# Kernel tuning notes

Hardware: AMD Instinct MI355X
Metric: run time of the kernel (lower is better)

Reference implementation:

```python
import jax, jax.numpy as jnp
import numpy as np

B, S = 32, 2048
D = 128      # embedding_dim
H = 256      # hidden_dim
K = 512      # codebook_size
RECON_COEF, COMMIT_COEF, VQ_COEF = 1.0, 0.15, 0.05


def _conv1d(x, w, b):
    # x: [B, Cin, S], w: [Cout, Cin, 3], 'SAME' padding (padding=1, k=3)
    y = jax.lax.conv_general_dilated(x, w, window_strides=(1,), padding='SAME',
                                     dimension_numbers=('NCH', 'OIH', 'NCH'))
    return y + b[None, :, None]


def _lrelu(x):
    return jnp.where(x >= 0, x, 0.2 * x)


def setup_inputs() -> dict:
    key = jax.random.key(0)
    ks = jax.random.split(key, 14)

    def w(k, shape, fan_in):
        bound = 1.0 / np.sqrt(fan_in)
        return jax.random.uniform(k, shape, jnp.float32, -bound, bound)

    return {
        'x': jax.random.normal(ks[0], (B, S), jnp.float32),
        'codebook': jax.random.normal(ks[1], (K, D), jnp.float32),
        'ew1': w(ks[2], (H, 1, 3), 1 * 3),  'eb1': w(ks[3], (H,), 1 * 3),
        'ew2': w(ks[4], (H, H, 3), H * 3),  'eb2': w(ks[5], (H,), H * 3),
        'ew3': w(ks[6], (D, H, 3), H * 3),  'eb3': w(ks[7], (D,), H * 3),
        'dw1': w(ks[8], (H, D, 3), D * 3),  'db1': w(ks[9], (H,), D * 3),
        'dw2': w(ks[10], (H, H, 3), H * 3), 'db2': w(ks[11], (H,), H * 3),
        'dw3': w(ks[12], (1, H, 3), H * 3), 'db3': w(ks[13], (1,), H * 3),
    }


def reference(x, codebook, ew1, eb1, ew2, eb2, ew3, eb3, dw1, db1, dw2, db2, dw3, db3):
    # ---- encode ----
    h = x[:, None, :]                                  # [B,1,S]
    h = _lrelu(_conv1d(h, ew1, eb1))
    h = _lrelu(_conv1d(h, ew2, eb2))
    z = _conv1d(h, ew3, eb3)                           # [B,D,S]

    # ---- vector quantize (eval mode: no EMA update) ----
    zt = jnp.transpose(z, (0, 2, 1))                   # [B,S,D]
    z_flat = zt.reshape(-1, D)                         # [B*S,D]
    # squared distances: |z|^2 + |c|^2 - 2 z c^T
    d = (jnp.sum(z_flat ** 2, axis=1, keepdims=True)
         + jnp.sum(codebook ** 2, axis=1)
         - 2.0 * z_flat @ codebook.T)                  # [B*S,K]
    idx = jnp.argmin(d, axis=1)                        # [B*S]
    z_q = codebook[idx].reshape(zt.shape)              # [B,S,D] (== one-hot @ codebook)

    vq_loss = jnp.mean((jax.lax.stop_gradient(zt) - z_q) ** 2) * VQ_COEF
    commitment_loss = jnp.mean((zt - jax.lax.stop_gradient(z_q)) ** 2) * COMMIT_COEF
    indices = idx.reshape(B, S)

    # ---- decode ----
    h = jnp.transpose(z_q, (0, 2, 1))                  # [B,D,S]
    h = _lrelu(_conv1d(h, dw1, db1))
    h = _lrelu(_conv1d(h, dw2, db2))
    x_recon = _conv1d(h, dw3, db3)[:, 0, :]            # [B,S]

    recon_loss = jnp.mean((x - x_recon) ** 2) * RECON_COEF
    loss = recon_loss + vq_loss + commitment_loss
    return x_recon, indices, loss, recon_loss, vq_loss, commitment_loss
```

## Files before the change

### kernel.cpp

```cpp
#include <hip/hip_runtime.h>
#include <float.h>

#define S_LEN 2048
#define BATCH 32
#define HCH   256
#define DCH   128
#define KCODES 512

typedef float  f32x4  __attribute__((ext_vector_type(4)));
typedef short  bf16x8 __attribute__((ext_vector_type(8)));
typedef short  short8 __attribute__((ext_vector_type(8)));

__device__ __forceinline__ float lrelu_f(float v) { return v >= 0.f ? v : 0.2f * v; }

__device__ __forceinline__ short f2bf(float f) {
    unsigned u = __float_as_uint(f);
    u = u + 0x7fffu + ((u >> 16) & 1u);
    return (short)(u >> 16);
}
__device__ __forceinline__ float bf2f(unsigned short u) {
    return __uint_as_float(((unsigned)u) << 16);
}

__global__ void prep_cb_split_kernel(const float* __restrict__ cb,
                                     short* __restrict__ cb_hi, short* __restrict__ cb_lo,
                                     float* __restrict__ cnorm) {
    int k = blockIdx.x * 256 + threadIdx.x;
    if (k < KCODES) {
        float s = 0.f;
        for (int d = 0; d < DCH; ++d) {
            float v = cb[k * DCH + d];
            s += v * v;
            short hi = f2bf(v);
            short lo = f2bf(v - bf2f((unsigned short)hi));
            cb_hi[k * DCH + d] = hi;
            cb_lo[k * DCH + d] = lo;
        }
        cnorm[k] = s;
    }
}

__global__ void prep_w_split_kernel(const float* __restrict__ Wsrc,
                                    short* __restrict__ Wh, short* __restrict__ Wl,
                                    int Cout, int Cin) {
    int i = blockIdx.x * 256 + threadIdx.x;
    int total = 3 * Cout * Cin;
    if (i < total) {
        int t = i / (Cout * Cin);
        int rem = i - t * Cout * Cin;
        int co = rem / Cin;
        int ci = rem - co * Cin;
        float v = Wsrc[(co * Cin + ci) * 3 + t];
        short hi = f2bf(v);
        Wh[i] = hi;
        Wl[i] = f2bf(v - bf2f((unsigned short)hi));
    }
}

__global__ void prep_wdec_kernel(const float* __restrict__ Wsrc, short* __restrict__ Wdst,
                                 int Cin) {
    int i = blockIdx.x * 256 + threadIdx.x;
    int total = 3 * 256 * Cin;
    if (i < total) {
        int t = i / (256 * Cin);
        int rem = i - t * 256 * Cin;
        int co = rem / Cin;
        int ci = rem - co * Cin;
        Wdst[i] = f2bf(Wsrc[(co * Cin + ci) * 3 + t]);
    }
}

__global__ void prep_w3t_kernel(const float* __restrict__ w3, float* __restrict__ w3t) {
    int i = blockIdx.x * 256 + threadIdx.x;
    if (i < 768) {
        int t = i / 256, ci = i - t * 256;
        w3t[i] = w3[ci * 3 + t];
    }
}

__global__ __launch_bounds__(256) void enc_conv1_cl_kernel(
        const float* __restrict__ x, short* __restrict__ h_hi, short* __restrict__ h_lo,
        const float* __restrict__ w, const float* __restrict__ bias) {
    __shared__ float ws[HCH * 3];
    __shared__ float bs[HCH];
    int tid = threadIdx.x;
    for (int i = tid; i < HCH * 3; i += 256) ws[i] = w[i];
    for (int i = tid; i < HCH; i += 256) bs[i] = bias[i];
    __syncthreads();
    int b = blockIdx.y;
    int s = blockIdx.x * 32 + (tid >> 3);
    int cch = tid & 7;
    const float* xb = x + (size_t)b * S_LEN;
    float xm = (s > 0) ? xb[s - 1] : 0.f;
    float x0 = xb[s];
    float xp = (s < S_LEN - 1) ? xb[s + 1] : 0.f;
    size_t base = ((size_t)(b * S_LEN + s)) * HCH + cch * 32;
#pragma unroll
    for (int cc = 0; cc < 4; ++cc) {
        short8 oh, ol;
#pragma unroll
        for (int e = 0; e < 8; ++e) {
            int co = cch * 32 + cc * 8 + e;
            float v = ws[co * 3 + 0] * xm + ws[co * 3 + 1] * x0 + ws[co * 3 + 2] * xp + bs[co];
            v = lrelu_f(v);
            short hi = f2bf(v);
            oh[e] = hi;
            ol[e] = f2bf(v - bf2f((unsigned short)hi));
        }
        *(short8*)(h_hi + base + cc * 8) = oh;
        *(short8*)(h_lo + base + cc * 8) = ol;
    }
}

__global__ __launch_bounds__(256) void conv_mfma_split(
        const short* __restrict__ in_hi, const short* __restrict__ in_lo,
        short* __restrict__ out_hi, short* __restrict__ out_lo,
        const short* __restrict__ wt_hi, const short* __restrict__ wt_lo,
        const float* __restrict__ bias, int Cin, int Cout, int do_lrelu) {
    __shared__ short smem[20800];
    short* Xh = smem;
    short* Xl = smem + 130 * 40;

    const int tid = threadIdx.x;
    const int lane = tid & 63;
    const int w = tid >> 6;
    const int m = lane & 15;
    const int q = lane >> 4;
    const int sOff = (w & 1) * 64;
    const int cOff = (w >> 1) * 64;
    const int b = blockIdx.z;
    const int s0 = blockIdx.x * 128;
    const int co0 = blockIdx.y * 128;

    f32x4 acc[4][4];
    f32x4 zero4 = {0.f, 0.f, 0.f, 0.f};
#pragma unroll
    for (int i = 0; i < 4; ++i)
#pragma unroll
        for (int j = 0; j < 4; ++j) acc[i][j] = zero4;

    const short* inhb = in_hi + (size_t)b * S_LEN * Cin;
    const short* inlb = in_lo + (size_t)b * S_LEN * Cin;

    for (int ci0 = 0; ci0 < Cin; ci0 += 32) {
        __syncthreads();
        for (int c = tid; c < 520; c += 256) {
            int r = c >> 2, part = c & 3;
            int s = s0 - 1 + r;
            float4 vh = make_float4(0.f, 0.f, 0.f, 0.f);
            float4 vl = vh;
            if (s >= 0 && s < S_LEN) {
                size_t goff = (size_t)s * Cin + ci0 + part * 8;
                vh = *(const float4*)(inhb + goff);
                vl = *(const float4*)(inlb + goff);
            }
            *(float4*)(Xh + r * 40 + part * 8) = vh;
            *(float4*)(Xl + r * 40 + part * 8) = vl;
        }
        __syncthreads();

#pragma unroll
        for (int t = 0; t < 3; ++t) {
            bf16x8 ah[4], al[4], bh[4], bl[4];
#pragma unroll
            for (int i = 0; i < 4; ++i) {
                int row = sOff + i * 16 + m + t;
                ah[i] = *(const bf16x8*)(Xh + row * 40 + q * 8);
                al[i] = *(const bf16x8*)(Xl + row * 40 + q * 8);
            }
#pragma unroll
            for (int j = 0; j < 4; ++j) {
                size_t woff = ((size_t)(t * Cout + co0 + cOff + j * 16 + m)) * Cin + ci0 + q * 8;
                bh[j] = *(const bf16x8*)(wt_hi + woff);
                bl[j] = *(const bf16x8*)(wt_lo + woff);
            }
#pragma unroll
            for (int i = 0; i < 4; ++i)
#pragma unroll
                for (int j = 0; j < 4; ++j) {
                    acc[i][j] = __builtin_amdgcn_mfma_f32_16x16x32_bf16(ah[i], bh[j], acc[i][j], 0, 0, 0);
                    acc[i][j] = __builtin_amdgcn_mfma_f32_16x16x32_bf16(ah[i], bl[j], acc[i][j], 0, 0, 0);
                    acc[i][j] = __builtin_amdgcn_mfma_f32_16x16x32_bf16(al[i], bh[j], acc[i][j], 0, 0, 0);
                }
        }
    }

    short* obH = smem + w * 5120;
    short* obL = obH + 2560;
#pragma unroll
    for (int p = 0; p < 2; ++p) {
        __syncthreads();
#pragma unroll
        for (int jj = 0; jj < 2; ++jj) {
            int j = 2 * p + jj;
            float bv = bias[co0 + cOff + j * 16 + m];
#pragma unroll
            for (int i = 0; i < 4; ++i) {
#pragma unroll
                for (int r = 0; r < 4; ++r) {
                    float val = acc[i][j][r] + bv;
                    if (do_lrelu) val = lrelu_f(val);
                    short hi = f2bf(val);
                    short lo = f2bf(val - bf2f((unsigned short)hi));
                    int row = i * 16 + q * 4 + r;
                    int col = jj * 16 + m;
                    obH[row * 40 + col] = hi;
                    obL[row * 40 + col] = lo;
                }
            }
        }
        __syncthreads();
        const int chunk = lane & 3;
        const int rsub = lane >> 2;
#pragma unroll
        for (int it = 0; it < 4; ++it) {
            int row = it * 16 + rsub;
            short8 vh = *(const short8*)(obH + row * 40 + chunk * 8);
            short8 vl = *(const short8*)(obL + row * 40 + chunk * 8);
            size_t goff = ((size_t)(b * S_LEN + s0 + sOff + row)) * Cout + co0 + cOff + p * 32 + chunk * 8;
            *(short8*)(out_hi + goff) = vh;
            *(short8*)(out_lo + goff) = vl;
        }
    }
}

__global__ __launch_bounds__(256) void vq_mfma_kernel(
        const short* __restrict__ z_hi, const short* __restrict__ z_lo,
        const short* __restrict__ cb_hi, const short* __restrict__ cb_lo,
        const float* __restrict__ cnorm, int* __restrict__ idx_out,
        float* __restrict__ idx_f_out) {
    __shared__ short smem[2 * 64 * 136];
    __shared__ float redv[64][4];
    __shared__ int   redi[64][4];
    short* Zh = smem;
    short* Zl = smem + 64 * 136;

    const int tid = threadIdx.x;
    const int lane = tid & 63;
    const int w = tid >> 6;
    const int m = lane & 15;
    const int q = lane >> 4;
    const int n0 = blockIdx.x * 64;

    for (int c = tid; c < 2048; c += 256) {
        int buf = c >> 10;
        int rem = c & 1023;
        int r = rem >> 4, part = rem & 15;
        size_t goff = (size_t)(n0 + r) * DCH + part * 8;
        float4 v = buf ? *(const float4*)(z_lo + goff) : *(const float4*)(z_hi + goff);
        *(float4*)((buf ? Zl : Zh) + r * 136 + part * 8) = v;
    }
    __syncthreads();

    float best[4][4];
    int besti[4][4];
#pragma unroll
    for (int i = 0; i < 4; ++i)
#pragma unroll
        for (int r = 0; r < 4; ++r) { best[i][r] = FLT_MAX; besti[i][r] = 0; }

    for (int k0 = 0; k0 < KCODES; k0 += 256) {
        f32x4 acc[4][4];
        f32x4 zero4 = {0.f, 0.f, 0.f, 0.f};
#pragma unroll
        for (int i = 0; i < 4; ++i)
#pragma unroll
            for (int j = 0; j < 4; ++j) acc[i][j] = zero4;

#pragma unroll
        for (int d0 = 0; d0 < DCH; d0 += 32) {
            bf16x8 ah[4], al[4], bh[4], bl[4];
#pragma unroll
            for (int i = 0; i < 4; ++i) {
                int row = i * 16 + m;
                ah[i] = *(const bf16x8*)(Zh + row * 136 + d0 + q * 8);
                al[i] = *(const bf16x8*)(Zl + row * 136 + d0 + q * 8);
            }
#pragma unroll
            for (int j = 0; j < 4; ++j) {
                size_t coff = (size_t)(k0 + w * 64 + j * 16 + m) * DCH + d0 + q * 8;
                bh[j] = *(const bf16x8*)(cb_hi + coff);
                bl[j] = *(const bf16x8*)(cb_lo + coff);
            }
#pragma unroll
            for (int i = 0; i < 4; ++i)
#pragma unroll
                for (int j = 0; j < 4; ++j) {
                    acc[i][j] = __builtin_amdgcn_mfma_f32_16x16x32_bf16(ah[i], bh[j], acc[i][j], 0, 0, 0);
                    acc[i][j] = __builtin_amdgcn_mfma_f32_16x16x32_bf16(ah[i], bl[j], acc[i][j], 0, 0, 0);
                    acc[i][j] = __builtin_amdgcn_mfma_f32_16x16x32_bf16(al[i], bh[j], acc[i][j], 0, 0, 0);
                }
        }
#pragma unroll
        for (int j = 0; j < 4; ++j) {
            int k = k0 + w * 64 + j * 16 + m;
            float cn = cnorm[k];
#pragma unroll
            for (int i = 0; i < 4; ++i)
#pragma unroll
                for (int r = 0; r < 4; ++r) {
                    float dv = cn - 2.f * acc[i][j][r];
                    if (dv < best[i][r]) { best[i][r] = dv; besti[i][r] = k; }
                }
        }
    }

#pragma unroll
    for (int mask = 1; mask < 16; mask <<= 1) {
#pragma unroll
        for (int i = 0; i < 4; ++i)
#pragma unroll
            for (int r = 0; r < 4; ++r) {
                float ov = __shfl_xor(best[i][r], mask);
                int oi = __shfl_xor(besti[i][r], mask);
                if (ov < best[i][r] || (ov == best[i][r] && oi < besti[i][r])) {
                    best[i][r] = ov; besti[i][r] = oi;
                }
            }
    }
    if (m == 0) {
#pragma unroll
        for (int i = 0; i < 4; ++i)
#pragma unroll
            for (int r = 0; r < 4; ++r) {
                int srow = i * 16 + q * 4 + r;
                redv[srow][w] = best[i][r];
                redi[srow][w] = besti[i][r];
            }
    }
    __syncthreads();
    if (tid < 64) {
        float bv = redv[tid][0];
        int bi = redi[tid][0];
#pragma unroll
        for (int w2 = 1; w2 < 4; ++w2) {
            float v = redv[tid][w2];
            int ii = redi[tid][w2];
            if (v < bv || (v == bv && ii < bi)) { bv = v; bi = ii; }
        }
        int n = n0 + tid;
        idx_out[n] = bi;
        idx_f_out[n] = (float)bi;
    }
}

__global__ __launch_bounds__(256) void gather_vqsum_kernel(
        const float* __restrict__ cb, const int* __restrict__ idxb,
        const short* __restrict__ z_hi, const short* __restrict__ z_lo,
        short* __restrict__ zq, float* __restrict__ acc_vq) {
    int tid = threadIdx.x;
    int b = blockIdx.y;
    int s = blockIdx.x * 32 + (tid >> 3);
    int dpart = tid & 7;
    int n = b * S_LEN + s;
    int k = idxb[n];
    const float* src = cb + (size_t)k * DCH + dpart * 16;
    size_t zoff = (size_t)n * DCH + dpart * 16;
    float sum = 0.f;
    short8 outv[2];
#pragma unroll
    for (int half = 0; half < 2; ++half) {
        float4 f0 = *(const float4*)(src + half * 8);
        float4 f1 = *(const float4*)(src + half * 8 + 4);
        bf16x8 zh = *(const bf16x8*)(z_hi + zoff + half * 8);
        bf16x8 zl = *(const bf16x8*)(z_lo + zoff + half * 8);
        float qv[8] = {f0.x, f0.y, f0.z, f0.w, f1.x, f1.y, f1.z, f1.w};
        short8 o;
#pragma unroll
        for (int e = 0; e < 8; ++e) {
            o[e] = f2bf(qv[e]);
            float zv = bf2f((unsigned short)zh[e]) + bf2f((unsigned short)zl[e]);
            float df = zv - qv[e];
            sum += df * df;
        }
        outv[half] = o;
    }
    *(short8*)(zq + zoff) = outv[0];
    *(short8*)(zq + zoff + 8) = outv[1];
    for (int off = 32; off > 0; off >>= 1) sum += __shfl_down(sum, off);
    __shared__ float wsum[4];
    if ((tid & 63) == 0) wsum[tid >> 6] = sum;
    __syncthreads();
    if (tid == 0) atomicAdd(acc_vq, wsum[0] + wsum[1] + wsum[2] + wsum[3]);
}

__global__ __launch_bounds__(256) void conv_mfma_cl(
        const short* __restrict__ in, short* __restrict__ out,
        const short* __restrict__ wt, const float* __restrict__ bias,
        int Cin) {
    __shared__ short smem[24672];
    short* Xs = smem;
    short* Ws = smem + 130 * 48;

    const int tid = threadIdx.x;
    const int lane = tid & 63;
    const int w = tid >> 6;
    const int m = lane & 15;
    const int q = lane >> 4;
    const int sOff = (w & 1) * 64;
    const int cOff = (w >> 1) * 64;
    const int b = blockIdx.z;
    const int s0 = blockIdx.x * 128;
    const int co0 = blockIdx.y * 128;

    f32x4 acc[4][4];
    f32x4 zero4 = {0.f, 0.f, 0.f, 0.f};
#pragma unroll
    for (int i = 0; i < 4; ++i)
#pragma unroll
        for (int j = 0; j < 4; ++j) acc[i][j] = zero4;

    const short* inb = in + (size_t)b * S_LEN * Cin;

    for (int ci0 = 0; ci0 < Cin; ci0 += 32) {
        __syncthreads();
        for (int c = tid; c < 520; c += 256) {
            int r = c >> 2, part = c & 3;
            int s = s0 - 1 + r;
            float4 v = make_float4(0.f, 0.f, 0.f, 0.f);
            if (s >= 0 && s < S_LEN)
                v = *(const float4*)(inb + (size_t)s * Cin + ci0 + part * 8);
            *(float4*)(Xs + r * 48 + part * 8) = v;
        }
        for (int c = tid; c < 1536; c += 256) {
            int t = c >> 9;
            int rem = c & 511;
            int cr = rem >> 2, part = rem & 3;
            float4 v = *(const float4*)(wt + ((size_t)(t * 256 + co0 + cr)) * Cin + ci0 + part * 8);
            *(float4*)(Ws + (t * 128 + cr) * 48 + part * 8) = v;
        }
        __syncthreads();

#pragma unroll
        for (int t = 0; t < 3; ++t) {
            bf16x8 a[4], bb[4];
#pragma unroll
            for (int i = 0; i < 4; ++i)
                a[i] = *(const bf16x8*)(Xs + (sOff + i * 16 + m + t) * 48 + q * 8);
#pragma unroll
            for (int j = 0; j < 4; ++j)
                bb[j] = *(const bf16x8*)(Ws + (t * 128 + cOff + j * 16 + m) * 48 + q * 8);
#pragma unroll
            for (int i = 0; i < 4; ++i)
#pragma unroll
                for (int j = 0; j < 4; ++j)
                    acc[i][j] = __builtin_amdgcn_mfma_f32_16x16x32_bf16(
                        a[i], bb[j], acc[i][j], 0, 0, 0);
        }
    }

    __syncthreads();

    short* ob = smem + w * (64 * 80);
#pragma unroll
    for (int j = 0; j < 4; ++j) {
        float bv = bias[co0 + cOff + j * 16 + m];
#pragma unroll
        for (int i = 0; i < 4; ++i) {
#pragma unroll
            for (int r = 0; r < 4; ++r) {
                float val = acc[i][j][r] + bv;
                val = lrelu_f(val);
                ob[(i * 16 + q * 4 + r) * 80 + j * 16 + m] = f2bf(val);
            }
        }
    }
    const int rsel = lane >> 3;
    const int off8 = (lane & 7) * 8;
#pragma unroll
    for (int pass = 0; pass < 8; ++pass) {
        int rr = pass * 8 + rsel;
        short8 v = *(const short8*)(ob + rr * 80 + off8);
        *(short8*)(out + ((size_t)(b * S_LEN + s0 + sOff + rr)) * 256 + co0 + cOff + off8) = v;
    }
}

__global__ __launch_bounds__(256) void dec_conv3_tiled_kernel(
        const short* __restrict__ h, const float* __restrict__ w3t,
        const float* __restrict__ b3, const float* __restrict__ x,
        float* __restrict__ xr, float* __restrict__ acc_recon) {
    __shared__ short Zs[66 * 264];
    __shared__ float ws[3 * 256];
    __shared__ float wsum[4];
    int tid = threadIdx.x;
    int b = blockIdx.y;
    int s0 = blockIdx.x * 64;
    const short* hb = h + (size_t)b * S_LEN * HCH;
    for (int i = tid; i < 768; i += 256) ws[i] = w3t[i];
    for (int c = tid; c < 2112; c += 256) {
        int r = c >> 5, part = c & 31;
        int g = s0 - 1 + r;
        short8 v = {0, 0, 0, 0, 0, 0, 0, 0};
        if (g >= 0 && g < S_LEN)
            v = *(const short8*)(hb + (size_t)g * HCH + part * 8);
        *(short8*)(Zs + r * 264 + part * 8) = v;
    }
    __syncthreads();

    int quarter = tid & 3;
    int sl = tid >> 2;
    float a0 = 0.f, a1 = 0.f, a2 = 0.f, a3 = 0.f;
#pragma unroll
    for (int t = 0; t < 3; ++t) {
        const short* zrow = Zs + (sl + t) * 264 + quarter * 64;
        const float* wrow = ws + t * 256 + quarter * 64;
#pragma unroll
        for (int c = 0; c < 8; ++c) {
            bf16x8 v = *(const bf16x8*)(zrow + c * 8);
            float4 w0 = *(const float4*)(wrow + c * 8);
            float4 w1 = *(const float4*)(wrow + c * 8 + 4);
            a0 = fmaf(w0.x, bf2f((unsigned short)v[0]), a0);
            a1 = fmaf(w0.y, bf2f((unsigned short)v[1]), a1);
            a2 = fmaf(w0.z, bf2f((unsigned short)v[2]), a2);
            a3 = fmaf(w0.w, bf2f((unsigned short)v[3]), a3);
            a0 = fmaf(w1.x, bf2f((unsigned short)v[4]), a0);
            a1 = fmaf(w1.y, bf2f((unsigned short)v[5]), a1);
            a2 = fmaf(w1.z, bf2f((unsigned short)v[6]), a2);
            a3 = fmaf(w1.w, bf2f((unsigned short)v[7]), a3);
        }
    }
    float acc = (a0 + a1) + (a2 + a3);
    acc += __shfl_xor(acc, 1);
    acc += __shfl_xor(acc, 2);
    float df2 = 0.f;
    if (quarter == 0) {
        int s = s0 + sl;
        float tot = acc + b3[0];
        xr[b * S_LEN + s] = tot;
        float df = x[b * S_LEN + s] - tot;
        df2 = df * df;
    }
    for (int off = 32; off > 0; off >>= 1) df2 += __shfl_down(df2, off);
    int lane = tid & 63, wv = tid >> 6;
    if (lane == 0) wsum[wv] = df2;
    __syncthreads();
    if (tid == 0) atomicAdd(acc_recon, wsum[0] + wsum[1] + wsum[2] + wsum[3]);
}

__global__ void finalize_kernel(const float* __restrict__ accs, float* __restrict__ out) {
    if (threadIdx.x == 0) {
        float vqm = accs[0] / ((float)BATCH * S_LEN * DCH);
        float rm  = accs[1] / ((float)BATCH * S_LEN);
        float vq_loss = vqm * 0.05f;
        float commit  = vqm * 0.15f;
        float recon   = rm * 1.0f;
        out[0] = recon + vq_loss + commit;
        out[1] = recon;
        out[2] = vq_loss;
        out[3] = commit;
    }
}

extern "C" void kernel_launch(void* const* d_in, const int* in_sizes, int n_in,
                              void* d_out, int out_size, void* d_ws, size_t ws_size,
                              hipStream_t stream) {
    const float* x    = (const float*)d_in[0];
    const float* cb   = (const float*)d_in[1];
    const float* ew1  = (const float*)d_in[2];
    const float* eb1  = (const float*)d_in[3];
    const float* ew2  = (const float*)d_in[4];
    const float* eb2  = (const float*)d_in[5];
    const float* ew3  = (const float*)d_in[6];
    const float* eb3  = (const float*)d_in[7];
    const float* dw1  = (const float*)d_in[8];
    const float* db1  = (const float*)d_in[9];
    const float* dw2  = (const float*)d_in[10];
    const float* db2  = (const float*)d_in[11];
    const float* dw3  = (const float*)d_in[12];
    const float* db3  = (const float*)d_in[13];

    float* out = (float*)d_out;
    float* xr    = out;
    float* idx_f = out + BATCH * S_LEN;
    float* loss_out = out + 2 * BATCH * S_LEN;

    const size_t NH = (size_t)BATCH * S_LEN * HCH;
    const size_t ND = (size_t)BATCH * S_LEN * DCH;

    short* sp = (short*)d_ws;
    short* h1_hi = sp;
    short* h1_lo = sp + NH;
    short* z_hi  = sp;
    short* z_lo  = sp + ND;
    short* h1d_bf = sp;
    short* h2_hi = sp + 2 * NH;
    short* h2_lo = sp + 3 * NH;
    short* zq_bf = sp + 2 * NH;
    short* h2d_bf = sp + 3 * NH;
    short* sm = sp + 4 * NH;
    short* cb_hi = sm; sm += KCODES * DCH;
    short* cb_lo = sm; sm += KCODES * DCH;
    short* w2_hi = sm; sm += 3 * HCH * HCH;
    short* w2_lo = sm; sm += 3 * HCH * HCH;
    short* w3_hi = sm; sm += 3 * DCH * HCH;
    short* w3_lo = sm; sm += 3 * DCH * HCH;
    short* wbf_d1 = sm; sm += 3 * 256 * DCH;
    short* wbf_d2 = sm; sm += 3 * 256 * HCH;
    float* cnorm = (float*)sm;
    int* idxb = (int*)(cnorm + KCODES);
    float* w3t = (float*)(idxb + BATCH * S_LEN);
    float* accs = w3t + 768;

    hipMemsetAsync(accs, 0, 2 * sizeof(float), stream);

    prep_cb_split_kernel<<<2, 256, 0, stream>>>(cb, cb_hi, cb_lo, cnorm);
    prep_w_split_kernel<<<(3 * HCH * HCH + 255) / 256, 256, 0, stream>>>(ew2, w2_hi, w2_lo, HCH, HCH);
    prep_w_split_kernel<<<(3 * DCH * HCH + 255) / 256, 256, 0, stream>>>(ew3, w3_hi, w3_lo, DCH, HCH);
    prep_wdec_kernel<<<(3 * 256 * DCH + 255) / 256, 256, 0, stream>>>(dw1, wbf_d1, DCH);
    prep_wdec_kernel<<<(3 * 256 * HCH + 255) / 256, 256, 0, stream>>>(dw2, wbf_d2, HCH);
    prep_w3t_kernel<<<3, 256, 0, stream>>>(dw3, w3t);

    enc_conv1_cl_kernel<<<dim3(S_LEN / 32, BATCH), 256, 0, stream>>>(x, h1_hi, h1_lo, ew1, eb1);
    conv_mfma_split<<<dim3(S_LEN / 128, HCH / 128, BATCH), 256, 0, stream>>>(
        h1_hi, h1_lo, h2_hi, h2_lo, w2_hi, w2_lo, eb2, HCH, HCH, 1);
    conv_mfma_split<<<dim3(S_LEN / 128, DCH / 128, BATCH), 256, 0, stream>>>(
        h2_hi, h2_lo, z_hi, z_lo, w3_hi, w3_lo, eb3, HCH, DCH, 0);

    vq_mfma_kernel<<<(BATCH * S_LEN) / 64, 256, 0, stream>>>(
        z_hi, z_lo, cb_hi, cb_lo, cnorm, idxb, idx_f);
    gather_vqsum_kernel<<<dim3(S_LEN / 32, BATCH), 256, 0, stream>>>(
        cb, idxb, z_hi, z_lo, zq_bf, accs);

    conv_mfma_cl<<<dim3(S_LEN / 128, 2, BATCH), 256, 0, stream>>>(
        zq_bf, h1d_bf, wbf_d1, db1, DCH);
    conv_mfma_cl<<<dim3(S_LEN / 128, 2, BATCH), 256, 0, stream>>>(
        h1d_bf, h2d_bf, wbf_d2, db2, HCH);
    dec_conv3_tiled_kernel<<<dim3(S_LEN / 64, BATCH), 256, 0, stream>>>(
        h2d_bf, w3t, db3, x, xr, accs + 1);

    finalize_kernel<<<1, 64, 0, stream>>>(accs, loss_out);
}
```

Baseline: 524.7 us.

## Shrink conv LDS footprint, widen K-chunk to 64, read weights directly from global

Both MFMA conv kernels now stage 64 input channels per iteration with a padded stride of 68, which halves the number of barrier-separated load phases. The conv_mfma_cl kernel no longer stages weights in LDS and reads them straight from global/L2, as the split kernel already did. The epilogues write one 16-column chunk at a time through a small per-wave buffer, and launch_bounds now request 4 blocks per CU. Together these cut shared memory use to raise occupancy, at the cost of more global weight traffic and possible register pressure under the tighter bound. The VQ kernel also issues its codebook global loads before the LDS loads to hide their latency.

```diff
diff --git a/kernel.cpp b/kernel.cpp
--- a/kernel.cpp
+++ b/kernel.cpp
@@ -112,14 +112,14 @@
     }
 }
 
-__global__ __launch_bounds__(256) void conv_mfma_split(
+__global__ __launch_bounds__(256, 4) void conv_mfma_split(
         const short* __restrict__ in_hi, const short* __restrict__ in_lo,
         short* __restrict__ out_hi, short* __restrict__ out_lo,
         const short* __restrict__ wt_hi, const short* __restrict__ wt_lo,
         const float* __restrict__ bias, int Cin, int Cout, int do_lrelu) {
-    __shared__ short smem[20800];
+    __shared__ short smem[17680];
     short* Xh = smem;
-    short* Xl = smem + 130 * 40;
+    short* Xl = smem + 130 * 68;
 
     const int tid = threadIdx.x;
     const int lane = tid & 63;
@@ -142,82 +142,81 @@
     const short* inhb = in_hi + (size_t)b * S_LEN * Cin;
     const short* inlb = in_lo + (size_t)b * S_LEN * Cin;
 
-    for (int ci0 = 0; ci0 < Cin; ci0 += 32) {
+    for (int ci0 = 0; ci0 < Cin; ci0 += 64) {
         __syncthreads();
-        for (int c = tid; c < 520; c += 256) {
-            int r = c >> 2, part = c & 3;
+        for (int c = tid; c < 2080; c += 256) {
+            int r = c >> 4;
+            int sub = c & 15;
+            int half = sub >> 3;
+            int part = sub & 7;
             int s = s0 - 1 + r;
-            float4 vh = make_float4(0.f, 0.f, 0.f, 0.f);
-            float4 vl = vh;
+            float4 v = make_float4(0.f, 0.f, 0.f, 0.f);
             if (s >= 0 && s < S_LEN) {
                 size_t goff = (size_t)s * Cin + ci0 + part * 8;
-                vh = *(const float4*)(inhb + goff);
-                vl = *(const float4*)(inlb + goff);
-            }
-            *(float4*)(Xh + r * 40 + part * 8) = vh;
-            *(float4*)(Xl + r * 40 + part * 8) = vl;
+                v = half ? *(const float4*)(inlb + goff) : *(const float4*)(inhb + goff);
+            }
+            *(float4*)((half ? Xl : Xh) + r * 68 + part * 8) = v;
         }
         __syncthreads();
 
 #pragma unroll
-        for (int t = 0; t < 3; ++t) {
-            bf16x8 ah[4], al[4], bh[4], bl[4];
-#pragma unroll
-            for (int i = 0; i < 4; ++i) {
-                int row = sOff + i * 16 + m + t;
-                ah[i] = *(const bf16x8*)(Xh + row * 40 + q * 8);
-                al[i] = *(const bf16x8*)(Xl + row * 40 + q * 8);
-            }
-#pragma unroll
-            for (int j = 0; j < 4; ++j) {
-                size_t woff = ((size_t)(t * Cout + co0 + cOff + j * 16 + m)) * Cin + ci0 + q * 8;
-                bh[j] = *(const bf16x8*)(wt_hi + woff);
-                bl[j] = *(const bf16x8*)(wt_lo + woff);
-            }
-#pragma unroll
-            for (int i = 0; i < 4; ++i)
+        for (int ks = 0; ks < 2; ++ks) {
+            const int kofs = ks * 32;
+#pragma unroll
+            for (int t = 0; t < 3; ++t) {
+                bf16x8 ah[4], al[4], bh[4], bl[4];
 #pragma unroll
                 for (int j = 0; j < 4; ++j) {
-                    acc[i][j] = __builtin_amdgcn_mfma_f32_16x16x32_bf16(ah[i], bh[j], acc[i][j], 0, 0, 0);
-                    acc[i][j] = __builtin_amdgcn_mfma_f32_16x16x32_bf16(ah[i], bl[j], acc[i][j], 0, 0, 0);
-                    acc[i][j] = __builtin_amdgcn_mfma_f32_16x16x32_bf16(al[i], bh[j], acc[i][j], 0, 0, 0);
+                    size_t woff = ((size_t)(t * Cout + co0 + cOff + j * 16 + m)) * Cin + ci0 + kofs + q * 8;
+                    bh[j] = *(const bf16x8*)(wt_hi + woff);
+                    bl[j] = *(const bf16x8*)(wt_lo + woff);
                 }
-        }
-    }
-
-    short* obH = smem + w * 5120;
-    short* obL = obH + 2560;
-#pragma unroll
-    for (int p = 0; p < 2; ++p) {
-        __syncthreads();
-#pragma unroll
-        for (int jj = 0; jj < 2; ++jj) {
-            int j = 2 * p + jj;
-            float bv = bias[co0 + cOff + j * 16 + m];
-#pragma unroll
-            for (int i = 0; i < 4; ++i) {
-#pragma unroll
-                for (int r = 0; r < 4; ++r) {
-                    float val = acc[i][j][r] + bv;
-                    if (do_lrelu) val = lrelu_f(val);
-                    short hi = f2bf(val);
-                    short lo = f2bf(val - bf2f((unsigned short)hi));
-                    int row = i * 16 + q * 4 + r;
-                    int col = jj * 16 + m;
-                    obH[row * 40 + col] = hi;
-                    obL[row * 40 + col] = lo;
+#pragma unroll
+                for (int i = 0; i < 4; ++i) {
+                    int row = sOff + i * 16 + m + t;
+                    ah[i] = *(const bf16x8*)(Xh + row * 68 + kofs + q * 8);
+                    al[i] = *(const bf16x8*)(Xl + row * 68 + kofs + q * 8);
                 }
-            }
-        }
-        __syncthreads();
-        const int chunk = lane & 3;
-        const int rsub = lane >> 2;
-#pragma unroll
-        for (int it = 0; it < 4; ++it) {
-            int row = it * 16 + rsub;
-            short8 vh = *(const short8*)(obH + row * 40 + chunk * 8);
-            short8 vl = *(const short8*)(obL + row * 40 + chunk * 8);
-            size_t goff = ((size_t)(b * S_LEN + s0 + sOff + row)) * Cout + co0 + cOff + p * 32 + chunk * 8;
+#pragma unroll
+                for (int i = 0; i < 4; ++i)
+#pragma unroll
+                    for (int j = 0; j < 4; ++j) {
+                        acc[i][j] = __builtin_amdgcn_mfma_f32_16x16x32_bf16(ah[i], bh[j], acc[i][j], 0, 0, 0);
+                        acc[i][j] = __builtin_amdgcn_mfma_f32_16x16x32_bf16(ah[i], bl[j], acc[i][j], 0, 0, 0);
+                        acc[i][j] = __builtin_amdgcn_mfma_f32_16x16x32_bf16(al[i], bh[j], acc[i][j], 0, 0, 0);
+                    }
+            }
+        }
+    }
+
+    __syncthreads();
+    short* obH = smem + w * 2560;
+    short* obL = obH + 1280;
+#pragma unroll
+    for (int j = 0; j < 4; ++j) {
+        float bv = bias[co0 + cOff + j * 16 + m];
+#pragma unroll
+        for (int i = 0; i < 4; ++i) {
+#pragma unroll
+            for (int r = 0; r < 4; ++r) {
+                float val = acc[i][j][r] + bv;
+                if (do_lrelu) val = lrelu_f(val);
+                short hi = f2bf(val);
+                short lo = f2bf(val - bf2f((unsigned short)hi));
+                int row = i * 16 + q * 4 + r;
+                obH[row * 20 + m] = hi;
+                obL[row * 20 + m] = lo;
+            }
+        }
+        const int colchunk = lane & 1;
+        const int rbase = lane >> 1;
+#pragma unroll
+        for (int it = 0; it < 2; ++it) {
+            int row = it * 32 + rbase;
+            short8 vh = *(const short8*)(obH + row * 20 + colchunk * 8);
+            short8 vl = *(const short8*)(obL + row * 20 + colchunk * 8);
+            size_t goff = ((size_t)(b * S_LEN + s0 + sOff + row)) * Cout
+                        + co0 + cOff + j * 16 + colchunk * 8;
             *(short8*)(out_hi + goff) = vh;
             *(short8*)(out_lo + goff) = vl;
         }
@@ -271,16 +270,16 @@
         for (int d0 = 0; d0 < DCH; d0 += 32) {
             bf16x8 ah[4], al[4], bh[4], bl[4];
 #pragma unroll
+            for (int j = 0; j < 4; ++j) {
+                size_t coff = (size_t)(k0 + w * 64 + j * 16 + m) * DCH + d0 + q * 8;
+                bh[j] = *(const bf16x8*)(cb_hi + coff);
+                bl[j] = *(const bf16x8*)(cb_lo + coff);
+            }
+#pragma unroll
             for (int i = 0; i < 4; ++i) {
                 int row = i * 16 + m;
                 ah[i] = *(const bf16x8*)(Zh + row * 136 + d0 + q * 8);
                 al[i] = *(const bf16x8*)(Zl + row * 136 + d0 + q * 8);
-            }
-#pragma unroll
-            for (int j = 0; j < 4; ++j) {
-                size_t coff = (size_t)(k0 + w * 64 + j * 16 + m) * DCH + d0 + q * 8;
-                bh[j] = *(const bf16x8*)(cb_hi + coff);
-                bl[j] = *(const bf16x8*)(cb_lo + coff);
             }
 #pragma unroll
             for (int i = 0; i < 4; ++i)
@@ -384,13 +383,12 @@
     if (tid == 0) atomicAdd(acc_vq, wsum[0] + wsum[1] + wsum[2] + wsum[3]);
 }
 
-__global__ __launch_bounds__(256) void conv_mfma_cl(
+__global__ __launch_bounds__(256, 4) void conv_mfma_cl(
         const short* __restrict__ in, short* __restrict__ out,
         const short* __restrict__ wt, const float* __restrict__ bias,
         int Cin) {
-    __shared__ short smem[24672];
+    __shared__ short smem[8840];
     short* Xs = smem;
-    short* Ws = smem + 130 * 48;
 
     const int tid = threadIdx.x;
     const int lane = tid & 63;
@@ -412,46 +410,43 @@
 
     const short* inb = in + (size_t)b * S_LEN * Cin;
 
-    for (int ci0 = 0; ci0 < Cin; ci0 += 32) {
+    for (int ci0 = 0; ci0 < Cin; ci0 += 64) {
         __syncthreads();
-        for (int c = tid; c < 520; c += 256) {
-            int r = c >> 2, part = c & 3;
+        for (int c = tid; c < 1040; c += 256) {
+            int r = c >> 3;
+            int part = c & 7;
             int s = s0 - 1 + r;
             float4 v = make_float4(0.f, 0.f, 0.f, 0.f);
             if (s >= 0 && s < S_LEN)
                 v = *(const float4*)(inb + (size_t)s * Cin + ci0 + part * 8);
-            *(float4*)(Xs + r * 48 + part * 8) = v;
-        }
-        for (int c = tid; c < 1536; c += 256) {
-            int t = c >> 9;
-            int rem = c & 511;
-            int cr = rem >> 2, part = rem & 3;
-            float4 v = *(const float4*)(wt + ((size_t)(t * 256 + co0 + cr)) * Cin + ci0 + part * 8);
-            *(float4*)(Ws + (t * 128 + cr) * 48 + part * 8) = v;
+            *(float4*)(Xs + r * 68 + part * 8) = v;
         }
         __syncthreads();
 
 #pragma unroll
-        for (int t = 0; t < 3; ++t) {
-            bf16x8 a[4], bb[4];
-#pragma unroll
-            for (int i = 0; i < 4; ++i)
-                a[i] = *(const bf16x8*)(Xs + (sOff + i * 16 + m + t) * 48 + q * 8);
-#pragma unroll
-            for (int j = 0; j < 4; ++j)
-                bb[j] = *(const bf16x8*)(Ws + (t * 128 + cOff + j * 16 + m) * 48 + q * 8);
-#pragma unroll
-            for (int i = 0; i < 4; ++i)
+        for (int ks = 0; ks < 2; ++ks) {
+            const int kofs = ks * 32;
+#pragma unroll
+            for (int t = 0; t < 3; ++t) {
+                bf16x8 a[4], bb[4];
 #pragma unroll
                 for (int j = 0; j < 4; ++j)
-                    acc[i][j] = __builtin_amdgcn_mfma_f32_16x16x32_bf16(
-                        a[i], bb[j], acc[i][j], 0, 0, 0);
-        }
-    }
-
-    __syncthreads();
-
-    short* ob = smem + w * (64 * 80);
+                    bb[j] = *(const bf16x8*)(wt + ((size_t)(t * 256 + co0 + cOff + j * 16 + m)) * Cin + ci0 + kofs + q * 8);
+#pragma unroll
+                for (int i = 0; i < 4; ++i)
+                    a[i] = *(const bf16x8*)(Xs + (sOff + i * 16 + m + t) * 68 + kofs + q * 8);
+#pragma unroll
+                for (int i = 0; i < 4; ++i)
+#pragma unroll
+                    for (int j = 0; j < 4; ++j)
+                        acc[i][j] = __builtin_amdgcn_mfma_f32_16x16x32_bf16(
+                            a[i], bb[j], acc[i][j], 0, 0, 0);
+            }
+        }
+    }
+
+    __syncthreads();
+    short* ob = smem + w * 1280;
 #pragma unroll
     for (int j = 0; j < 4; ++j) {
         float bv = bias[co0 + cOff + j * 16 + m];
@@ -461,17 +456,19 @@
             for (int r = 0; r < 4; ++r) {
                 float val = acc[i][j][r] + bv;
                 val = lrelu_f(val);
-                ob[(i * 16 + q * 4 + r) * 80 + j * 16 + m] = f2bf(val);
-            }
-        }
-    }
-    const int rsel = lane >> 3;
-    const int off8 = (lane & 7) * 8;
-#pragma unroll
-    for (int pass = 0; pass < 8; ++pass) {
-        int rr = pass * 8 + rsel;
-        short8 v = *(const short8*)(ob + rr * 80 + off8);
-        *(short8*)(out + ((size_t)(b * S_LEN + s0 + sOff + rr)) * 256 + co0 + cOff + off8) = v;
+                ob[(i * 16 + q * 4 + r) * 20 + m] = f2bf(val);
+            }
+        }
+        const int colchunk = lane & 1;
+        const int rbase = lane >> 1;
+#pragma unroll
+        for (int it = 0; it < 2; ++it) {
+            int row = it * 32 + rbase;
+            short8 v = *(const short8*)(ob + row * 20 + colchunk * 8);
+            size_t goff = ((size_t)(b * S_LEN + s0 + sOff + row)) * 256
+                        + co0 + cOff + j * 16 + colchunk * 8;
+            *(short8*)(out + goff) = v;
+        }
     }
 }
 
```

New measurement: 655.9 us. +25.0%, slower.
